# Optimization experiments

Hardware: AMD Instinct MI355X
Metric: run time of the kernel (lower is better)

The kernel has to match this reference:

```python
import jax, jax.numpy as jnp
import numpy as np

D_MODEL = 1024
N_HEADS = 16
D_KV = 64
NUM_BUCKETS = 32
MAX_DISTANCE = 128


def _relative_position_bucket(seq_len, num_buckets=NUM_BUCKETS, max_distance=MAX_DISTANCE):
    # bidirectional=True path of T5 bucketing
    ctx = jnp.arange(seq_len, dtype=jnp.int32)[:, None]
    mem = jnp.arange(seq_len, dtype=jnp.int32)[None, :]
    rel = mem - ctx  # [S, S]
    nb = num_buckets // 2
    buckets = (rel > 0).astype(jnp.int32) * nb
    rel = jnp.abs(rel)
    max_exact = nb // 2
    is_small = rel < max_exact
    # guard log(0); those entries are overridden by is_small anyway
    rel_f = jnp.maximum(rel, 1).astype(jnp.float32)
    rel_large = max_exact + (
        jnp.log(rel_f / max_exact) / np.log(max_distance / max_exact) * (nb - max_exact)
    ).astype(jnp.int32)
    rel_large = jnp.minimum(rel_large, nb - 1)
    return buckets + jnp.where(is_small, rel, rel_large)  # [S, S] int32


def setup_inputs() -> dict:
    key = jax.random.key(0)
    ks = jax.random.split(key, 11)
    B, S = 4, 2048
    hidden_states = jax.random.normal(ks[0], (B, S, D_MODEL), dtype=jnp.float32)
    attention_masks = jnp.zeros((B, 1, S, S), dtype=jnp.float32)
    w = lambda k: jax.random.normal(k, (D_MODEL, D_MODEL), dtype=jnp.float32) * 0.02
    b = lambda k: jax.random.normal(k, (D_MODEL,), dtype=jnp.float32) * 0.02
    rel_emb = jax.random.normal(ks[9], (NUM_BUCKETS, N_HEADS), dtype=jnp.float32) * 0.02
    return {
        "hidden_states": hidden_states,
        "attention_masks": attention_masks,
        "Wq": w(ks[1]), "bq": b(ks[2]),
        "Wk": w(ks[3]), "bk": b(ks[4]),
        "Wv": w(ks[5]), "bv": b(ks[6]),
        "Wo": w(ks[7]), "bo": b(ks[8]),
        "rel_emb": rel_emb,
    }


def reference(hidden_states, attention_masks, Wq, bq, Wk, bk, Wv, bv, Wo, bo, rel_emb):
    B, S, _ = hidden_states.shape

    def shape_heads(x):  # [B,S,D] -> [B,H,S,dk]
        return x.reshape(B, S, N_HEADS, D_KV).transpose(0, 2, 1, 3)

    q = shape_heads(hidden_states @ Wq.T + bq)
    k = shape_heads(hidden_states @ Wk.T + bk)
    v = shape_heads(hidden_states @ Wv.T + bv)

    scores = jnp.einsum("bhqd,bhkd->bhqk", q, k)  # [B,H,S,S]

    buckets = _relative_position_bucket(S)  # [S,S]
    position_bias = rel_emb[buckets].transpose(2, 0, 1)[None]  # [1,H,S,S]
    masks = position_bias + attention_masks  # broadcast -> [B,H,S,S]
    scores = scores + masks

    # NOTE: original scales by d_kv**2 (not sqrt), after mask addition
    attn = jax.nn.softmax(scores / float(D_KV ** 2), axis=-1)

    out = jnp.einsum("bhqk,bhkd->bhqd", attn, v)
    out = out.transpose(0, 2, 1, 3).reshape(B, S, D_MODEL)
    out = out @ Wo.T + bo
    return (out, masks)
```

## Files before the change

kernel.cpp:

```cpp
#include <hip/hip_runtime.h>
#include <cmath>


typedef __attribute__((ext_vector_type(8))) short bf16x8;
typedef __attribute__((ext_vector_type(4))) float f32x4;
typedef __attribute__((ext_vector_type(8))) unsigned short u16x8;

#define MFMA16(a, b, c) __builtin_amdgcn_mfma_f32_16x16x32_bf16((a), (b), (c), 0, 0, 0)

#define ASYNC_COPY16(g, l)                                                              \
  __builtin_amdgcn_global_load_lds((const __attribute__((address_space(1))) void*)(g),  \
                                   (__attribute__((address_space(3))) void*)(l), 16, 0, 0)

__device__ __forceinline__ unsigned short f2bf(float f) {
  unsigned u = __float_as_uint(f);
  u += 0x7FFFu + ((u >> 16) & 1u);
  return (unsigned short)(u >> 16);
}
__device__ __forceinline__ float bf2f(unsigned short u) {
  return __uint_as_float(((unsigned)u) << 16);
}

__device__ __forceinline__ int t5_bucket(int rel) {
  int bkt = (rel > 0) ? 16 : 0;
  int d = (rel < 0) ? -rel : rel;
  int v;
  if (d < 8) v = d;
  else if (d < 12) v = 8;
  else if (d < 16) v = 9;
  else if (d < 23) v = 10;
  else if (d < 32) v = 11;
  else if (d < 46) v = 12;
  else if (d < 64) v = 13;
  else if (d < 91) v = 14;
  else v = 15;
  return bkt + v;
}

struct Cast5Args {
  const float* src[5];
  unsigned short* dst[5];
};
__global__ __launch_bounds__(256) void cast5_kernel(Cast5Args a) {
  int i = (blockIdx.x * 256 + threadIdx.x) * 4;
  int seg, loc;
  if (i < 8388608) { seg = 0; loc = i; }
  else { seg = 1 + ((i - 8388608) >> 20); loc = (i - 8388608) & 1048575; }
  float4 v = *(const float4*)(a.src[seg] + loc);
  ushort4 o;
  o.x = f2bf(v.x); o.y = f2bf(v.y); o.z = f2bf(v.z); o.w = f2bf(v.w);
  *(ushort4*)(a.dst[seg] + loc) = o;
}

__device__ __forceinline__ void gemm_core(const unsigned short* __restrict__ A,
                                          const unsigned short* __restrict__ Bt,
                                          const float* __restrict__ bias,
                                          void* __restrict__ Cout, int M, int N, int K,
                                          int epi, short* sh) {
  short* As = sh;
  short* Bs = sh + 128 * 64;
  const int lane = threadIdx.x & 63;
  const int wave = threadIdx.x >> 6;
  const int l15 = lane & 15, g = lane >> 4;
  const int m0 = blockIdx.x * 128;
  const int n0 = blockIdx.y * 128;
  const int wr = wave >> 1, wc = wave & 1;

  f32x4 acc[4][4] = {};

  const int srow_in = lane >> 3;
  const int spu = lane & 7;

  for (int k0 = 0; k0 < K; k0 += 64) {
#pragma unroll
    for (int q = 0; q < 4; ++q) {
      const int rbase = (wave * 4 + q) * 8;
      const int row = rbase + srow_in;
      const int usrc = spu ^ (row & 7);
      ASYNC_COPY16(A + (size_t)(m0 + row) * K + k0 + usrc * 8, As + rbase * 64);
      ASYNC_COPY16(Bt + (size_t)(n0 + row) * K + k0 + usrc * 8, Bs + rbase * 64);
    }
    __syncthreads();

#pragma unroll
    for (int kk = 0; kk < 2; ++kk) {
      bf16x8 af[4], bfr[4];
#pragma unroll
      for (int mi = 0; mi < 4; ++mi) {
        int row = wr * 64 + mi * 16 + l15;
        int pu = (kk * 4 + g) ^ (row & 7);
        af[mi] = *(const bf16x8*)(As + row * 64 + pu * 8);
      }
#pragma unroll
      for (int ni = 0; ni < 4; ++ni) {
        int row = wc * 64 + ni * 16 + l15;
        int pu = (kk * 4 + g) ^ (row & 7);
        bfr[ni] = *(const bf16x8*)(Bs + row * 64 + pu * 8);
      }
#pragma unroll
      for (int mi = 0; mi < 4; ++mi)
#pragma unroll
        for (int ni = 0; ni < 4; ++ni)
          acc[mi][ni] = MFMA16(af[mi], bfr[ni], acc[mi][ni]);
    }
    __syncthreads();
  }

  float bvv[4];
#pragma unroll
  for (int ni = 0; ni < 4; ++ni) bvv[ni] = bias[n0 + wc * 64 + ni * 16 + l15];

  if (epi == 0) {
    float* shf = (float*)sh;
#pragma unroll
    for (int p = 0; p < 2; ++p) {
      if (p) __syncthreads();
      if (wr == p) {
#pragma unroll
        for (int mi = 0; mi < 4; ++mi) {
#pragma unroll
          for (int ni = 0; ni < 4; ++ni) {
            int c = wc * 64 + ni * 16 + l15;
#pragma unroll
            for (int r = 0; r < 4; ++r) {
              int m = mi * 16 + (g << 2) + r;
              shf[m * 128 + ((((c >> 2) ^ (m & 7)) << 2) | (c & 3))] =
                  acc[mi][ni][r] + bvv[ni];
            }
          }
        }
      }
      __syncthreads();
      {
        int row = threadIdx.x >> 5;
        int u = threadIdx.x & 31;
#pragma unroll
        for (int k = 0; k < 8; ++k) {
          int rr = row + (k << 3);
          int pu = u ^ (rr & 7);
          f32x4 v = *(const f32x4*)(shf + rr * 128 + (pu << 2));
          *(f32x4*)((float*)Cout + (size_t)(m0 + p * 64 + rr) * N + n0 + (u << 2)) = v;
        }
      }
    }
  } else if (epi == 1) {
#pragma unroll
    for (int mi = 0; mi < 4; ++mi) {
      int ml = wr * 64 + mi * 16 + (g << 2);
#pragma unroll
      for (int ni = 0; ni < 4; ++ni) {
        int c = wc * 64 + ni * 16 + l15;
#pragma unroll
        for (int r = 0; r < 4; ++r) {
          int m = ml + r;
          int pc = (((c >> 3) ^ (m & 7)) << 3) | (c & 7);
          sh[m * 128 + pc] = (short)f2bf(acc[mi][ni][r] + bvv[ni]);
        }
      }
    }
    __syncthreads();
    {
      int m = threadIdx.x >> 1, half = threadIdx.x & 1;
      unsigned short* dst = (unsigned short*)Cout + (size_t)(m0 + m) * N + n0 + half * 64;
#pragma unroll
      for (int uu = 0; uu < 8; ++uu) {
        int u = half * 8 + uu;
        int pu = u ^ (m & 7);
        *(u16x8*)(dst + uu * 8) = *(const u16x8*)(sh + m * 128 + pu * 8);
      }
    }
  } else {
#pragma unroll
    for (int mi = 0; mi < 4; ++mi) {
      int ml = wr * 64 + mi * 16 + (g << 2);
#pragma unroll
      for (int ni = 0; ni < 4; ++ni) {
        int c = wc * 64 + ni * 16 + l15;
#pragma unroll
        for (int r = 0; r < 4; ++r) {
          int s = ml + r;
          int ps = (((s >> 3) ^ (c & 7)) << 3) | (s & 7);
          sh[c * 128 + ps] = (short)f2bf(acc[mi][ni][r] + bvv[ni]);
        }
      }
    }
    __syncthreads();
    {
      int c = threadIdx.x >> 1, half = threadIdx.x & 1;
      int col = n0 + c;
      int mb = m0 >> 11, ml = m0 & 2047;
      unsigned short* dst =
          (unsigned short*)Cout + (((size_t)(mb * 1024 + col)) << 11) + ml + half * 64;
#pragma unroll
      for (int uu = 0; uu < 8; ++uu) {
        int u = half * 8 + uu;
        int pu = u ^ (c & 7);
        *(u16x8*)(dst + uu * 8) = *(const u16x8*)(sh + c * 128 + pu * 8);
      }
    }
  }
}

struct QKVArgs {
  const unsigned short* A;
  const unsigned short* Bt[3];
  const float* bias[3];
  unsigned short* out[3];
};
__global__ __launch_bounds__(256) void qkv_gemm(QKVArgs a) {
  __shared__ __align__(16) short sh[2 * 128 * 64];
  const int z = blockIdx.z;
  gemm_core(a.A, a.Bt[z], a.bias[z], a.out[z], 8192, 1024, 1024, z == 2 ? 2 : 1, sh);
}

__global__ __launch_bounds__(256) void gemm_f32(const unsigned short* A,
                                                const unsigned short* Bt, const float* bias,
                                                float* Cout) {
  __shared__ __align__(16) short sh[2 * 128 * 64];
  gemm_core(A, Bt, bias, Cout, 8192, 1024, 1024, 0, sh);
}

template <int WM>
__global__ __launch_bounds__(512) void attn_fused(const unsigned short* __restrict__ Qg,
                                                  const unsigned short* __restrict__ Kg,
                                                  const unsigned short* __restrict__ Vtg,
                                                  const float* __restrict__ am,
                                                  const float* __restrict__ rel_emb,
                                                  unsigned short* __restrict__ Og,
                                                  float* __restrict__ mout) {
  const int bh = blockIdx.x;
  const int b = bh >> 4, h = bh & 15;
  const int q0 = blockIdx.y << 7;
  const int tid = threadIdx.x;
  const int lane = tid & 63, wave = tid >> 6;
  const int l15 = lane & 15, g = lane >> 4;

  __shared__ __align__(16) short Ks[64 * 72];
  __shared__ __align__(16) short Vt[64 * 72];
  __shared__ unsigned short pbr[2176];
  __shared__ __align__(16) unsigned short msPl[128 * 72];
  short* Qs = (short*)msPl;

  for (int t = tid; t < 2176; t += 512)
    pbr[t] = f2bf(rel_emb[t5_bucket(t - 127 - q0) * 16 + h]);

  const size_t base = ((size_t)b * 2048) * 1024 + h * 64;
  const size_t vtbase = (size_t)bh << 17;

  {
    int row = tid >> 2, cu = (tid & 3) << 4;
    const unsigned short* src = Qg + base + (size_t)(q0 + row) * 1024 + cu;
    u16x8 v0 = *(const u16x8*)src;
    u16x8 v1 = *(const u16x8*)(src + 8);
    *(u16x8*)(Qs + row * 72 + cu) = v0;
    *(u16x8*)(Qs + row * 72 + cu + 8) = v1;
  }
  __syncthreads();

  bf16x8 qf[2];
  {
    int row = (wave << 4) + l15;
    const short* p = Qs + row * 72 + (g << 3);
    qf[0] = *(const bf16x8*)p;
    qf[1] = *(const bf16x8*)(p + 32);
  }

  f32x4 acc[4] = {};
  f32x4 acc1 = {};
  const bf16x8 onesf = {16256, 16256, 16256, 16256, 16256, 16256, 16256, 16256};
  const int ilbase = (wave << 4) + (g << 2);
  const float SC = 1.442695041f / 4096.0f;

  const int srowK = tid >> 3;
  const int scuK = (tid & 7) << 3;
  const int mrow = tid >> 4;
  const int mf4 = tid & 15;

  for (int kt = 0; kt < 32; ++kt) {
    const int j0 = kt << 6;
    __syncthreads();
    {
      const unsigned short* ks = Kg + base + (size_t)(j0 + srowK) * 1024 + scuK;
      *(u16x8*)(Ks + srowK * 72 + scuK) = *(const u16x8*)ks;
      const unsigned short* vs = Vtg + vtbase + ((size_t)srowK << 11) + j0 + scuK;
      *(u16x8*)(Vt + srowK * 72 + scuK) = *(const u16x8*)vs;
    }
    f32x4 mreg[4];
#pragma unroll
    for (int p = 0; p < 4; ++p) {
      const int row = p * 32 + mrow;
      const int j = j0 + (mf4 << 2);
      f32x4 a = *(const f32x4*)(am + ((size_t)b * 2048 + q0 + row) * 2048 + j);
      const int pidx = j - row + 127;
      f32x4 m;
      m[0] = bf2f(pbr[pidx + 0]) + a[0];
      m[1] = bf2f(pbr[pidx + 1]) + a[1];
      m[2] = bf2f(pbr[pidx + 2]) + a[2];
      m[3] = bf2f(pbr[pidx + 3]) + a[3];
      mreg[p] = m;
      ushort4 mb;
      mb.x = f2bf(m[0]); mb.y = f2bf(m[1]); mb.z = f2bf(m[2]); mb.w = f2bf(m[3]);
      *(ushort4*)(msPl + row * 72 + (mf4 << 2)) = mb;
    }
    __syncthreads();

    if (WM) {
#pragma unroll
      for (int p = 0; p < 4; ++p) {
        const int row = p * 32 + mrow;
        f32x4* dst =
            (f32x4*)(mout + ((size_t)bh * 2048 + q0 + row) * 2048 + j0 + (mf4 << 2));
        __builtin_nontemporal_store(mreg[p], dst);
      }
    }

    f32x4 sacc[4] = {};
#pragma unroll
    for (int kk = 0; kk < 2; ++kk) {
      const int koff = (kk << 5) + (g << 3);
#pragma unroll
      for (int fj = 0; fj < 4; ++fj) {
        bf16x8 kf = *(const bf16x8*)(Ks + ((fj << 4) + l15) * 72 + koff);
        sacc[fj] = MFMA16(qf[kk], kf, sacc[fj]);
      }
    }

#pragma unroll
    for (int fj = 0; fj < 4; ++fj) {
      const int jl = (fj << 4) + l15;
#pragma unroll
      for (int r = 0; r < 4; ++r) {
        const int il = (wave << 4) + (g << 2) + r;
        float mval = bf2f(msPl[il * 72 + jl]);
        float p = exp2f((sacc[fj][r] + mval) * SC);
        msPl[il * 72 + jl] = f2bf(p);
      }
    }

#pragma unroll
    for (int kk = 0; kk < 2; ++kk) {
      const int koff = (kk << 5) + (g << 3);
      bf16x8 pf = *(const bf16x8*)((const short*)msPl + ((wave << 4) + l15) * 72 + koff);
      acc1 = MFMA16(pf, onesf, acc1);
#pragma unroll
      for (int fd = 0; fd < 4; ++fd) {
        bf16x8 vf = *(const bf16x8*)(Vt + ((fd << 4) + l15) * 72 + koff);
        acc[fd] = MFMA16(pf, vf, acc[fd]);
      }
    }
  }

#pragma unroll
  for (int fd = 0; fd < 4; ++fd) {
    int d = (fd << 4) + l15;
#pragma unroll
    for (int r = 0; r < 4; ++r) {
      float o = acc[fd][r] / acc1[r];
      Og[base + (size_t)(q0 + ilbase + r) * 1024 + d] = f2bf(o);
    }
  }
}

__global__ __launch_bounds__(256) void masks_kernel(const float* __restrict__ am,
                                                    const float* __restrict__ rel_emb,
                                                    float* __restrict__ mout) {
  const int bi = blockIdx.x;
  const int b = bi >> 11, i = bi & 2047;
  __shared__ float amrow[2048];
  __shared__ float remb[512];
  __shared__ unsigned char bkt[2048];
  for (int t = threadIdx.x; t < 512; t += 256) remb[t] = rel_emb[t];
  const float* arow = am + ((size_t)b * 2048 + i) * 2048;
  for (int t = threadIdx.x; t < 512; t += 256)
    *(float4*)(amrow + (t << 2)) = *(const float4*)(arow + (t << 2));
  for (int j = threadIdx.x; j < 2048; j += 256)
    bkt[j] = (unsigned char)t5_bucket(j - i);
  __syncthreads();
  for (int h = 0; h < 16; ++h) {
    float* dst = mout + (((size_t)(b * 16 + h)) * 2048 + i) * 2048;
    for (int t = threadIdx.x; t < 512; t += 256) {
      int j = t << 2;
      f32x4 o;
      o[0] = remb[(bkt[j + 0] << 4) + h] + amrow[j + 0];
      o[1] = remb[(bkt[j + 1] << 4) + h] + amrow[j + 1];
      o[2] = remb[(bkt[j + 2] << 4) + h] + amrow[j + 2];
      o[3] = remb[(bkt[j + 3] << 4) + h] + amrow[j + 3];
      __builtin_nontemporal_store(o, (f32x4*)(dst + j));
    }
  }
}

extern "C" void kernel_launch(void* const* d_in, const int* in_sizes, int n_in,
                              void* d_out, int out_size, void* d_ws, size_t ws_size,
                              hipStream_t stream) {
  const float* hs  = (const float*)d_in[0];
  const float* am  = (const float*)d_in[1];
  const float* Wq  = (const float*)d_in[2];
  const float* bq  = (const float*)d_in[3];
  const float* Wk  = (const float*)d_in[4];
  const float* bk  = (const float*)d_in[5];
  const float* Wv  = (const float*)d_in[6];
  const float* bv  = (const float*)d_in[7];
  const float* Wo  = (const float*)d_in[8];
  const float* bo  = (const float*)d_in[9];
  const float* rel = (const float*)d_in[10];

  float* out = (float*)d_out;
  float* mout = out + (size_t)8388608;

  const bool fused = ws_size >= (size_t)69206016;

  unsigned short *hsb, *wqb, *wkb, *wvb, *wob, *qb, *kb, *vtb, *aob;
  if (fused) {
    char* W = (char*)d_ws;
    qb  = (unsigned short*)(W);
    kb  = (unsigned short*)(W + 16777216);
    vtb = (unsigned short*)(W + 33554432);
    aob = (unsigned short*)(W + 50331648);
    wob = (unsigned short*)(W + 67108864);
    char* SB = (char*)mout;
    hsb = (unsigned short*)(SB);
    wqb = (unsigned short*)(SB + 16777216);
    wkb = (unsigned short*)(SB + 18874368);
    wvb = (unsigned short*)(SB + 20971520);
  } else {
    char* SB = (char*)mout;
    hsb = (unsigned short*)(SB);
    wqb = (unsigned short*)(SB + 16777216);
    wkb = (unsigned short*)(SB + 18874368);
    wvb = (unsigned short*)(SB + 20971520);
    wob = (unsigned short*)(SB + 23068672);
    qb  = (unsigned short*)(SB + 25165824);
    kb  = (unsigned short*)(SB + 41943040);
    vtb = (unsigned short*)(SB + 58720256);
    aob = (unsigned short*)(SB + 75497472);
  }

  Cast5Args ca;
  ca.src[0] = hs;  ca.dst[0] = hsb;
  ca.src[1] = Wq;  ca.dst[1] = wqb;
  ca.src[2] = Wk;  ca.dst[2] = wkb;
  ca.src[3] = Wv;  ca.dst[3] = wvb;
  ca.src[4] = Wo;  ca.dst[4] = wob;
  cast5_kernel<<<12288, 256, 0, stream>>>(ca);

  QKVArgs qa;
  qa.A = hsb;
  qa.Bt[0] = wqb;  qa.bias[0] = bq;  qa.out[0] = qb;
  qa.Bt[1] = wkb;  qa.bias[1] = bk;  qa.out[1] = kb;
  qa.Bt[2] = wvb;  qa.bias[2] = bv;  qa.out[2] = vtb;
  qkv_gemm<<<dim3(64, 8, 3), 256, 0, stream>>>(qa);

  if (fused) {
    attn_fused<1><<<dim3(64, 16), 512, 0, stream>>>(qb, kb, vtb, am, rel, aob, mout);
  } else {
    attn_fused<0><<<dim3(64, 16), 512, 0, stream>>>(qb, kb, vtb, am, rel, aob, mout);
  }

  gemm_f32<<<dim3(64, 8), 256, 0, stream>>>(aob, wob, bo, out);

  if (!fused) masks_kernel<<<8192, 256, 0, stream>>>(am, rel, mout);
}
```

Measured before the change: 403.6 us.

## Double attention query tile to 256 rows per block for K/V reuse

Each attention block now handles 256 query rows instead of 128, with each wave processing two 16-row groups, halving the grid. This halves K/V tile reloads and per-block setup, at the cost of more registers and LDS per block. The mask values are also kept in registers as bf16 and widened back to fp32 for the mask output, which reduces register pressure but rounds the stored mask output to bf16 precision.

```diff
diff --git a/kernel.cpp b/kernel.cpp
--- a/kernel.cpp
+++ b/kernel.cpp
@@ -230,45 +230,44 @@
                                                   float* __restrict__ mout) {
   const int bh = blockIdx.x;
   const int b = bh >> 4, h = bh & 15;
-  const int q0 = blockIdx.y << 7;
+  const int q0 = blockIdx.y << 8;
   const int tid = threadIdx.x;
   const int lane = tid & 63, wave = tid >> 6;
   const int l15 = lane & 15, g = lane >> 4;
 
   __shared__ __align__(16) short Ks[64 * 72];
   __shared__ __align__(16) short Vt[64 * 72];
-  __shared__ unsigned short pbr[2176];
-  __shared__ __align__(16) unsigned short msPl[128 * 72];
+  __shared__ unsigned short pbr[2304];
+  __shared__ __align__(16) unsigned short msPl[256 * 72];
   short* Qs = (short*)msPl;
 
-  for (int t = tid; t < 2176; t += 512)
-    pbr[t] = f2bf(rel_emb[t5_bucket(t - 127 - q0) * 16 + h]);
+  for (int t = tid; t < 2304; t += 512)
+    pbr[t] = f2bf(rel_emb[t5_bucket(t - 255 - q0) * 16 + h]);
 
   const size_t base = ((size_t)b * 2048) * 1024 + h * 64;
   const size_t vtbase = (size_t)bh << 17;
 
   {
-    int row = tid >> 2, cu = (tid & 3) << 4;
+    int row = tid >> 1, cu = (tid & 1) << 5;
     const unsigned short* src = Qg + base + (size_t)(q0 + row) * 1024 + cu;
-    u16x8 v0 = *(const u16x8*)src;
-    u16x8 v1 = *(const u16x8*)(src + 8);
-    *(u16x8*)(Qs + row * 72 + cu) = v0;
-    *(u16x8*)(Qs + row * 72 + cu + 8) = v1;
+#pragma unroll
+    for (int e = 0; e < 4; ++e)
+      *(u16x8*)(Qs + row * 72 + cu + e * 8) = *(const u16x8*)(src + e * 8);
   }
   __syncthreads();
 
-  bf16x8 qf[2];
-  {
-    int row = (wave << 4) + l15;
+  bf16x8 qf[2][2];
+#pragma unroll
+  for (int gr = 0; gr < 2; ++gr) {
+    int row = (wave << 5) + (gr << 4) + l15;
     const short* p = Qs + row * 72 + (g << 3);
-    qf[0] = *(const bf16x8*)p;
-    qf[1] = *(const bf16x8*)(p + 32);
-  }
-
-  f32x4 acc[4] = {};
-  f32x4 acc1 = {};
+    qf[gr][0] = *(const bf16x8*)p;
+    qf[gr][1] = *(const bf16x8*)(p + 32);
+  }
+
+  f32x4 acc[2][4] = {};
+  f32x4 acc1[2] = {};
   const bf16x8 onesf = {16256, 16256, 16256, 16256, 16256, 16256, 16256, 16256};
-  const int ilbase = (wave << 4) + (g << 2);
   const float SC = 1.442695041f / 4096.0f;
 
   const int srowK = tid >> 3;
@@ -285,78 +284,90 @@
       const unsigned short* vs = Vtg + vtbase + ((size_t)srowK << 11) + j0 + scuK;
       *(u16x8*)(Vt + srowK * 72 + scuK) = *(const u16x8*)vs;
     }
-    f32x4 mreg[4];
-#pragma unroll
-    for (int p = 0; p < 4; ++p) {
-      const int row = p * 32 + mrow;
+    ushort4 mbreg[8];
+#pragma unroll
+    for (int p = 0; p < 8; ++p) {
+      const int row = (p << 5) + mrow;
       const int j = j0 + (mf4 << 2);
       f32x4 a = *(const f32x4*)(am + ((size_t)b * 2048 + q0 + row) * 2048 + j);
-      const int pidx = j - row + 127;
-      f32x4 m;
-      m[0] = bf2f(pbr[pidx + 0]) + a[0];
-      m[1] = bf2f(pbr[pidx + 1]) + a[1];
-      m[2] = bf2f(pbr[pidx + 2]) + a[2];
-      m[3] = bf2f(pbr[pidx + 3]) + a[3];
-      mreg[p] = m;
+      const int pidx = j - row + 255;
       ushort4 mb;
-      mb.x = f2bf(m[0]); mb.y = f2bf(m[1]); mb.z = f2bf(m[2]); mb.w = f2bf(m[3]);
+      mb.x = f2bf(bf2f(pbr[pidx + 0]) + a[0]);
+      mb.y = f2bf(bf2f(pbr[pidx + 1]) + a[1]);
+      mb.z = f2bf(bf2f(pbr[pidx + 2]) + a[2]);
+      mb.w = f2bf(bf2f(pbr[pidx + 3]) + a[3]);
+      mbreg[p] = mb;
       *(ushort4*)(msPl + row * 72 + (mf4 << 2)) = mb;
     }
     __syncthreads();
 
     if (WM) {
 #pragma unroll
-      for (int p = 0; p < 4; ++p) {
-        const int row = p * 32 + mrow;
+      for (int p = 0; p < 8; ++p) {
+        const int row = (p << 5) + mrow;
+        f32x4 m;
+        m[0] = bf2f(mbreg[p].x);
+        m[1] = bf2f(mbreg[p].y);
+        m[2] = bf2f(mbreg[p].z);
+        m[3] = bf2f(mbreg[p].w);
         f32x4* dst =
             (f32x4*)(mout + ((size_t)bh * 2048 + q0 + row) * 2048 + j0 + (mf4 << 2));
-        __builtin_nontemporal_store(mreg[p], dst);
-      }
-    }
-
-    f32x4 sacc[4] = {};
-#pragma unroll
-    for (int kk = 0; kk < 2; ++kk) {
-      const int koff = (kk << 5) + (g << 3);
+        __builtin_nontemporal_store(m, dst);
+      }
+    }
+
+#pragma unroll
+    for (int gr = 0; gr < 2; ++gr) {
+      f32x4 sacc[4] = {};
+#pragma unroll
+      for (int kk = 0; kk < 2; ++kk) {
+        const int koff = (kk << 5) + (g << 3);
+#pragma unroll
+        for (int fj = 0; fj < 4; ++fj) {
+          bf16x8 kf = *(const bf16x8*)(Ks + ((fj << 4) + l15) * 72 + koff);
+          sacc[fj] = MFMA16(qf[gr][kk], kf, sacc[fj]);
+        }
+      }
+
+      const int ilb = (wave << 5) + (gr << 4) + (g << 2);
 #pragma unroll
       for (int fj = 0; fj < 4; ++fj) {
-        bf16x8 kf = *(const bf16x8*)(Ks + ((fj << 4) + l15) * 72 + koff);
-        sacc[fj] = MFMA16(qf[kk], kf, sacc[fj]);
-      }
-    }
-
-#pragma unroll
-    for (int fj = 0; fj < 4; ++fj) {
-      const int jl = (fj << 4) + l15;
+        const int jl = (fj << 4) + l15;
+#pragma unroll
+        for (int r = 0; r < 4; ++r) {
+          const int il = ilb + r;
+          float mval = bf2f(msPl[il * 72 + jl]);
+          float p = exp2f((sacc[fj][r] + mval) * SC);
+          msPl[il * 72 + jl] = f2bf(p);
+        }
+      }
+
+#pragma unroll
+      for (int kk = 0; kk < 2; ++kk) {
+        const int koff = (kk << 5) + (g << 3);
+        bf16x8 pf = *(const bf16x8*)((const short*)msPl +
+                                     ((wave << 5) + (gr << 4) + l15) * 72 + koff);
+        acc1[gr] = MFMA16(pf, onesf, acc1[gr]);
+#pragma unroll
+        for (int fd = 0; fd < 4; ++fd) {
+          bf16x8 vf = *(const bf16x8*)(Vt + ((fd << 4) + l15) * 72 + koff);
+          acc[gr][fd] = MFMA16(pf, vf, acc[gr][fd]);
+        }
+      }
+    }
+  }
+
+#pragma unroll
+  for (int gr = 0; gr < 2; ++gr) {
+    const int ilb = (wave << 5) + (gr << 4) + (g << 2);
+#pragma unroll
+    for (int fd = 0; fd < 4; ++fd) {
+      int d = (fd << 4) + l15;
 #pragma unroll
       for (int r = 0; r < 4; ++r) {
-        const int il = (wave << 4) + (g << 2) + r;
-        float mval = bf2f(msPl[il * 72 + jl]);
-        float p = exp2f((sacc[fj][r] + mval) * SC);
-        msPl[il * 72 + jl] = f2bf(p);
-      }
-    }
-
-#pragma unroll
-    for (int kk = 0; kk < 2; ++kk) {
-      const int koff = (kk << 5) + (g << 3);
-      bf16x8 pf = *(const bf16x8*)((const short*)msPl + ((wave << 4) + l15) * 72 + koff);
-      acc1 = MFMA16(pf, onesf, acc1);
-#pragma unroll
-      for (int fd = 0; fd < 4; ++fd) {
-        bf16x8 vf = *(const bf16x8*)(Vt + ((fd << 4) + l15) * 72 + koff);
-        acc[fd] = MFMA16(pf, vf, acc[fd]);
-      }
-    }
-  }
-
-#pragma unroll
-  for (int fd = 0; fd < 4; ++fd) {
-    int d = (fd << 4) + l15;
-#pragma unroll
-    for (int r = 0; r < 4; ++r) {
-      float o = acc[fd][r] / acc1[r];
-      Og[base + (size_t)(q0 + ilbase + r) * 1024 + d] = f2bf(o);
+        float o = acc[gr][fd][r] / acc1[gr][r];
+        Og[base + (size_t)(q0 + ilb + r) * 1024 + d] = f2bf(o);
+      }
     }
   }
 }
@@ -452,9 +463,9 @@
   qkv_gemm<<<dim3(64, 8, 3), 256, 0, stream>>>(qa);
 
   if (fused) {
-    attn_fused<1><<<dim3(64, 16), 512, 0, stream>>>(qb, kb, vtb, am, rel, aob, mout);
+    attn_fused<1><<<dim3(64, 8), 512, 0, stream>>>(qb, kb, vtb, am, rel, aob, mout);
   } else {
-    attn_fused<0><<<dim3(64, 16), 512, 0, stream>>>(qb, kb, vtb, am, rel, aob, mout);
+    attn_fused<0><<<dim3(64, 8), 512, 0, stream>>>(qb, kb, vtb, am, rel, aob, mout);
   }
 
   gemm_f32<<<dim3(64, 8), 256, 0, stream>>>(aob, wob, bo, out);
```

After: 413.4 us. +2.4%, slower.
